# Kernel tuning notes

Measured on AMD Instinct MI355X. Metric: run time of the kernel, lower is better.

## Reference

```python
import jax, jax.numpy as jnp
import numpy as np

N = 100000   # number of orientation vectors
MUL = 128    # multiplicity per output irrep


def _cg_tensors():
    # Clebsch-Gordan (wigner-3j style) tensors for 1o x 1o -> 0e, 1e, 2e
    # l=1 basis in e3nn real-SH order: index 0=y, 1=z, 2=x
    Y, Z, X = 0, 1, 2
    # l_out = 0: identity / sqrt(3)
    c0 = np.zeros((3, 3, 1), np.float32)
    for i in range(3):
        c0[i, i, 0] = 1.0 / np.sqrt(3.0)
    # l_out = 1: Levi-Civita / sqrt(6) (cyclic in (y,z,x) = cyclic in (x,y,z))
    c1 = np.zeros((3, 3, 3), np.float32)
    s = 1.0 / np.sqrt(6.0)
    for (i, j, k) in [(0, 1, 2), (1, 2, 0), (2, 0, 1)]:
        c1[i, j, k] = s
        c1[j, i, k] = -s
    # l_out = 2: symmetric traceless part, m = -2..2 -> (xy, yz, 2z^2-x^2-y^2, zx, x^2-y^2)
    a = 1.0 / np.sqrt(10.0)
    c2 = np.zeros((3, 3, 5), np.float32)
    c2[X, Y, 0] = c2[Y, X, 0] = a
    c2[Y, Z, 1] = c2[Z, Y, 1] = a
    c2[Z, Z, 2] = 2.0 * a / np.sqrt(3.0)
    c2[Y, Y, 2] = -a / np.sqrt(3.0)
    c2[X, X, 2] = -a / np.sqrt(3.0)
    c2[Z, X, 3] = c2[X, Z, 3] = a
    c2[X, X, 4] = a
    c2[Y, Y, 4] = -a
    return jnp.asarray(c0), jnp.asarray(c1), jnp.asarray(c2)

_CG = _cg_tensors()
# e3nn path weights: irrep_normalization='component', path_normalization='element'
# -> alpha = (2*l_out+1) / (mul1*mul2) = 2l+1, coefficient = sqrt(alpha)
_PW = (1.0, 3.0 ** 0.5, 5.0 ** 0.5)


def setup_inputs() -> dict:
    key = jax.random.key(0)
    k1, k2 = jax.random.split(key)
    ori = jax.random.normal(k1, (N, 3), dtype=jnp.float32)
    weights = jax.random.normal(k2, (3 * MUL,), dtype=jnp.float32)
    return {"ori": ori, "weights": weights}


def reference(ori, weights):
    # TensorProduct(1o, 1o -> 128x0e+128x1e+128x2e), 'uvw' paths, shared weights.
    w = weights.reshape(3, MUL)  # one (1,1,MUL) weight block per path
    n = ori.shape[0]
    outs = []
    for p, (cg, pw) in enumerate(zip(_CG, _PW)):
        t = jnp.einsum('ni,nj,ijk->nk', ori, ori, cg)      # [N, 2l+1]
        blk = pw * jnp.einsum('nk,w->nwk', t, w[p])        # [N, MUL, 2l+1]
        outs.append(blk.reshape(n, -1))
    return jnp.concatenate(outs, axis=-1)  # [N, MUL*(1+3+5)]
```

## Files before the change

### kernel.cpp

```cpp
#include <hip/hip_runtime.h>


#define THREADS 256
#define CPR 144
#define GRID 1017
#define BATCH 8
#define NB 7
#define RPG (BATCH * NB)

typedef float v4f __attribute__((ext_vector_type(4)));

__device__ __forceinline__ void emit_row(v4f* __restrict__ out4, int n, int c,
                                         float vy, float vz, float vx,
                                         const float coef[8], const int sel[8]) {
    const float xx = vx * vx, yy = vy * vy, zz = vz * vz;
    const float s0 = (xx + yy + zz) * 0.57735026918962576f;
    const float s1 = 1.41421356237309505f * (vx * vy);
    const float s2 = 1.41421356237309505f * (vy * vz);
    const float s3 = 0.40824829046386302f * (2.0f * zz - xx - yy);
    const float s4 = 1.41421356237309505f * (vz * vx);
    const float s5 = 0.70710678118654752f * (xx - yy);
    float r[8];
#pragma unroll
    for (int i = 0; i < 8; ++i) {
        float t = s0;
        t = (sel[i] == 1) ? s1 : t;
        t = (sel[i] == 2) ? s2 : t;
        t = (sel[i] == 3) ? s3 : t;
        t = (sel[i] == 4) ? s4 : t;
        t = (sel[i] == 5) ? s5 : t;
        r[i] = coef[i] * t;
    }
    const size_t ob = (size_t)n * (2 * CPR) + c;
    v4f a; a.x = r[0]; a.y = r[1]; a.z = r[2]; a.w = r[3];
    v4f b; b.x = r[4]; b.y = r[5]; b.z = r[6]; b.w = r[7];
    __builtin_nontemporal_store(a, &out4[ob]);
    __builtin_nontemporal_store(b, &out4[ob + CPR]);
}

__global__ __launch_bounds__(THREADS, 4) void ori_embed_kernel(
    const float* __restrict__ ori,
    const float* __restrict__ weights,
    float* __restrict__ out,
    int n_rows)
{
    const int tid = blockIdx.x * THREADS + threadIdx.x;
    const int c = tid % CPR;
    const int g = tid / CPR;
    const int r0 = g * RPG;
    if (r0 >= n_rows) return;

    float coef[8];
    int sel[8];
#pragma unroll
    for (int i = 0; i < 8; ++i) {
        const int col = (i < 4) ? (4 * c + i) : (576 + 4 * c + (i - 4));
        if (col < 128)      { coef[i] = weights[col];  sel[i] = 0; }
        else if (col < 512) { coef[i] = 0.0f;          sel[i] = 0; }
        else { const int j = col - 512;
               coef[i] = weights[256 + j / 5];         sel[i] = 1 + j % 5; }
    }

    v4f* __restrict__ out4 = reinterpret_cast<v4f*>(out);
    const v4f* __restrict__ src = reinterpret_cast<const v4f*>(ori);

    const int nb = min(NB, (n_rows - r0) / BATCH);
    const int base = 42 * g;

    v4f cur[6], nxt[6];
    if (nb > 0) {
#pragma unroll
        for (int k = 0; k < 6; ++k) cur[k] = src[base + k];
    }
    for (int b = 0; b < nb; ++b) {
        const bool more = (b + 1 < nb);
        if (more) {
#pragma unroll
            for (int k = 0; k < 6; ++k) nxt[k] = src[base + 6 * (b + 1) + k];
        }
        const float* f = reinterpret_cast<const float*>(cur);
        const int rb = r0 + b * BATCH;
#pragma unroll
        for (int j = 0; j < BATCH; ++j) {
            emit_row(out4, rb + j, c, f[3 * j + 0], f[3 * j + 1], f[3 * j + 2],
                     coef, sel);
        }
        if (more) {
#pragma unroll
            for (int k = 0; k < 6; ++k) cur[k] = nxt[k];
        }
    }

    const int rend = min(r0 + RPG, n_rows);
    for (int n = r0 + nb * BATCH; n < rend; ++n) {
        emit_row(out4, n, c, ori[3 * n + 0], ori[3 * n + 1], ori[3 * n + 2],
                 coef, sel);
    }
}

extern "C" void kernel_launch(void* const* d_in, const int* in_sizes, int n_in,
                              void* d_out, int out_size, void* d_ws, size_t ws_size,
                              hipStream_t stream) {
    const float* ori = (const float*)d_in[0];
    const float* weights = (const float*)d_in[1];
    float* out = (float*)d_out;
    const int n_rows = in_sizes[0] / 3;

    hipLaunchKernelGGL(ori_embed_kernel, dim3(GRID), dim3(THREADS), 0, stream,
                       ori, weights, out, n_rows);
}
```

Baseline: 96.15 us.

## Split zero l=1 block into separate fill kernel and shrink compute kernel

Writes the identically-zero l=1 output region with a dedicated zero-fill kernel, and narrows the compute kernel to only the l=0 and l=2 chunks with two float4 stores per thread per row. Nontemporal stores are replaced by regular stores and the grid sizes are retuned. The aim is to stop spending compute threads on zero columns, at the cost of an extra kernel launch and a different write pattern across two kernels.

```diff
diff --git a/kernel.cpp b/kernel.cpp
--- a/kernel.cpp
+++ b/kernel.cpp
@@ -1,16 +1,33 @@
 #include <hip/hip_runtime.h>
 
 
-#define THREADS 256
-#define CPR 144
-#define GRID 1017
-#define BATCH 8
-#define NB 7
-#define RPG (BATCH * NB)
-
 typedef float v4f __attribute__((ext_vector_type(4)));
 
-__device__ __forceinline__ void emit_row(v4f* __restrict__ out4, int n, int c,
+#define ZT 256
+#define ZGRID 513
+
+__global__ __launch_bounds__(ZT) void zero_fill_kernel(float* __restrict__ out,
+                                                       int n_rows)
+{
+    v4f* __restrict__ out4 = reinterpret_cast<v4f*>(out);
+    const int tid = blockIdx.x * ZT + threadIdx.x;
+    const int cic = tid % 96;
+    int row = tid / 96;
+    const int rstride = (ZGRID * ZT) / 96;
+    v4f z = {0.0f, 0.0f, 0.0f, 0.0f};
+    for (; row < n_rows; row += rstride)
+        out4[(size_t)row * 288 + 32 + cic] = z;
+}
+
+#define BT 256
+#define BCPR 96
+#define BGRID 939
+#define BRPG 40
+#define BBATCH 8
+#define BNB 5
+
+__device__ __forceinline__ void emit_row(v4f* __restrict__ out4, int n,
+                                         int g1, int g2,
                                          float vy, float vz, float vx,
                                          const float coef[8], const int sel[8]) {
     const float xx = vx * vx, yy = vy * vy, zz = vz * vz;
@@ -31,41 +48,47 @@
         t = (sel[i] == 5) ? s5 : t;
         r[i] = coef[i] * t;
     }
-    const size_t ob = (size_t)n * (2 * CPR) + c;
-    v4f a; a.x = r[0]; a.y = r[1]; a.z = r[2]; a.w = r[3];
-    v4f b; b.x = r[4]; b.y = r[5]; b.z = r[6]; b.w = r[7];
-    __builtin_nontemporal_store(a, &out4[ob]);
-    __builtin_nontemporal_store(b, &out4[ob + CPR]);
+    const size_t rb = (size_t)n * 288;
+    v4f a = {r[0], r[1], r[2], r[3]};
+    v4f b = {r[4], r[5], r[6], r[7]};
+    out4[rb + g1] = a;
+    out4[rb + g2] = b;
 }
 
-__global__ __launch_bounds__(THREADS, 4) void ori_embed_kernel(
+__global__ __launch_bounds__(BT, 4) void compute_kernel(
     const float* __restrict__ ori,
     const float* __restrict__ weights,
     float* __restrict__ out,
     int n_rows)
 {
-    const int tid = blockIdx.x * THREADS + threadIdx.x;
-    const int c = tid % CPR;
-    const int g = tid / CPR;
-    const int r0 = g * RPG;
+    const int tid = blockIdx.x * BT + threadIdx.x;
+    const int c = tid % BCPR;
+    const int g = tid / BCPR;
+    const int r0 = g * BRPG;
     if (r0 >= n_rows) return;
 
     float coef[8];
     int sel[8];
+    int gch[2];
 #pragma unroll
-    for (int i = 0; i < 8; ++i) {
-        const int col = (i < 4) ? (4 * c + i) : (576 + 4 * c + (i - 4));
-        if (col < 128)      { coef[i] = weights[col];  sel[i] = 0; }
-        else if (col < 512) { coef[i] = 0.0f;          sel[i] = 0; }
-        else { const int j = col - 512;
-               coef[i] = weights[256 + j / 5];         sel[i] = 1 + j % 5; }
+    for (int h = 0; h < 2; ++h) {
+        const int z = c + 96 * h;
+        const int col0 = (z < 32) ? 4 * z : 4 * z + 384;
+        gch[h] = (z < 32) ? z : z + 96;
+#pragma unroll
+        for (int k = 0; k < 4; ++k) {
+            const int col = col0 + k;
+            if (col < 128) { coef[4 * h + k] = weights[col];  sel[4 * h + k] = 0; }
+            else { const int j = col - 512;
+                   coef[4 * h + k] = weights[256 + j / 5];    sel[4 * h + k] = 1 + j % 5; }
+        }
     }
 
     v4f* __restrict__ out4 = reinterpret_cast<v4f*>(out);
     const v4f* __restrict__ src = reinterpret_cast<const v4f*>(ori);
 
-    const int nb = min(NB, (n_rows - r0) / BATCH);
-    const int base = 42 * g;
+    const int nb = min(BNB, (n_rows - r0) / BBATCH);
+    const int base = 30 * g;
 
     v4f cur[6], nxt[6];
     if (nb > 0) {
@@ -79,23 +102,21 @@
             for (int k = 0; k < 6; ++k) nxt[k] = src[base + 6 * (b + 1) + k];
         }
         const float* f = reinterpret_cast<const float*>(cur);
-        const int rb = r0 + b * BATCH;
+        const int rb = r0 + b * BBATCH;
 #pragma unroll
-        for (int j = 0; j < BATCH; ++j) {
-            emit_row(out4, rb + j, c, f[3 * j + 0], f[3 * j + 1], f[3 * j + 2],
-                     coef, sel);
-        }
+        for (int j = 0; j < BBATCH; ++j)
+            emit_row(out4, rb + j, gch[0], gch[1],
+                     f[3 * j + 0], f[3 * j + 1], f[3 * j + 2], coef, sel);
         if (more) {
 #pragma unroll
             for (int k = 0; k < 6; ++k) cur[k] = nxt[k];
         }
     }
 
-    const int rend = min(r0 + RPG, n_rows);
-    for (int n = r0 + nb * BATCH; n < rend; ++n) {
-        emit_row(out4, n, c, ori[3 * n + 0], ori[3 * n + 1], ori[3 * n + 2],
-                 coef, sel);
-    }
+    const int rend = min(r0 + BRPG, n_rows);
+    for (int n = r0 + nb * BBATCH; n < rend; ++n)
+        emit_row(out4, n, gch[0], gch[1],
+                 ori[3 * n + 0], ori[3 * n + 1], ori[3 * n + 2], coef, sel);
 }
 
 extern "C" void kernel_launch(void* const* d_in, const int* in_sizes, int n_in,
@@ -106,6 +127,8 @@
     float* out = (float*)d_out;
     const int n_rows = in_sizes[0] / 3;
 
-    hipLaunchKernelGGL(ori_embed_kernel, dim3(GRID), dim3(THREADS), 0, stream,
+    hipLaunchKernelGGL(zero_fill_kernel, dim3(ZGRID), dim3(ZT), 0, stream,
+                       out, n_rows);
+    hipLaunchKernelGGL(compute_kernel, dim3(BGRID), dim3(BT), 0, stream,
                        ori, weights, out, n_rows);
 }
```

After: 98.16 us. 1.02x slower.
